# Performance work log

Measured on AMD Instinct MI355X. Metric: run time of the kernel, lower is better.

The kernel has to match this reference:

```python
import jax, jax.numpy as jnp
import numpy as np

WINDOW = 5  # len_sort_window in the original module


def setup_inputs() -> dict:
    key = jax.random.key(0)
    k1, k2, k3 = jax.random.split(key, 3)
    B, L, D = 8, 4000, 512  # L divisible by WINDOW, D < L
    q = jax.random.normal(k1, (B, L, D), dtype=jnp.float32)
    k = jax.random.normal(k2, (B, L, D), dtype=jnp.float32)
    v = jax.random.normal(k3, (B, L, D), dtype=jnp.float32)
    return {"q": q, "k": k, "v": v}


def reference(q, k, v):
    # q, k are unused by the original forward.
    B, L, D = v.shape
    t = jnp.arange(L)          # sequence positions
    s = jnp.arange(D)          # per-feature cyclic shift amount (= feature index)
    # Shift feature i left by i: shifted[:, t, i] = v[:, (t + i) % L, i]
    idx_fwd = (t[:, None] + s[None, :]) % L            # [L, D]
    v_shift = jnp.take_along_axis(v, idx_fwd[None, :, :], axis=1)  # [B, L, D]
    # Sort within fixed non-overlapping windows of size WINDOW along the seq axis.
    v_sorted = jnp.sort(v_shift.reshape(B, L // WINDOW, WINDOW, D), axis=2)
    v_sorted = v_sorted.reshape(B, L, D)
    # Unshift feature i right by i: out[:, t, i] = v_sorted[:, (t - i) % L, i]
    idx_bwd = (t[:, None] - s[None, :]) % L            # [L, D]
    return jnp.take_along_axis(v_sorted, idx_bwd[None, :, :], axis=1)
```

## Files before the change

### kernel.cpp

```cpp
#include <hip/hip_runtime.h>


constexpr int L   = 4000;
constexpr int D   = 512;
constexpr int NW  = L / 5;
constexpr int WPB = 2;
constexpr int NBX = NW / WPB;

typedef float f4 __attribute__((ext_vector_type(4)));

#define CE(a, b) { float lo_ = fminf(a, b); float hi_ = fmaxf(a, b); (a) = lo_; (b) = hi_; }

__global__ __launch_bounds__(256, 4)
void swd18_asmld(const float* __restrict__ v, float* __restrict__ out) {
    const int nwg = gridDim.x * gridDim.y;
    const int lid = blockIdx.x + gridDim.x * blockIdx.y;
    const int qq  = nwg >> 3;
    const int xcd = lid & 7;
    const int pos = lid >> 3;
    const int nid = xcd * qq + pos;

    const int b  = nid / NBX;
    const int bx = nid % NBX;

    const int w  = WPB * bx + (threadIdx.x >> 7);
    const int q  = threadIdx.x & 127;
    const int c0 = q << 2;
    const int R0 = 5 * w;

    const f4* __restrict__ vb4 = (const f4*)(v   + (size_t)b * (L * D));
    f4*       __restrict__ ob4 = (f4*)      (out + (size_t)b * (L * D));

    f4 in[14];
#pragma unroll
    for (int r = 0; r < 14; ++r) {
        int row = R0 - 5 + r;
        if (row < 0)  row += L;
        if (row >= L) row -= L;
        const f4* p = vb4 + (size_t)row * (D / 4) + q;
        asm volatile("global_load_dwordx4 %0, %1, off"
                     : "=&v"(in[r]) : "v"(p));
    }
    asm volatile("s_waitcnt vmcnt(0)" ::: "memory");
    __builtin_amdgcn_sched_barrier(0);

    const int rc0 = c0 % 5;
    f4 o0, o1, o2, o3, o4;

#define COMP(J, F) do {                                                         \
    int rcj = rc0 + (J); if (rcj >= 5) rcj -= 5;                                \
    const bool e0 = rcj == 0, e1 = rcj == 1, e2 = rcj == 2, e3 = rcj == 3;      \
    float A0 = e0 ? in[0].F : e1 ? in[1].F : e2 ? in[2].F : e3 ? in[3].F : in[4].F;   \
    float A1 = e0 ? in[1].F : e1 ? in[2].F : e2 ? in[3].F : e3 ? in[4].F : in[5].F;   \
    float A2 = e0 ? in[2].F : e1 ? in[3].F : e2 ? in[4].F : e3 ? in[5].F : in[6].F;   \
    float A3 = e0 ? in[3].F : e1 ? in[4].F : e2 ? in[5].F : e3 ? in[6].F : in[7].F;   \
    float A4 = e0 ? in[4].F : e1 ? in[5].F : e2 ? in[6].F : e3 ? in[7].F : in[8].F;   \
    float B0 = e0 ? in[5].F : e1 ? in[6].F : e2 ? in[7].F : e3 ? in[8].F : in[9].F;   \
    float B1 = e0 ? in[6].F : e1 ? in[7].F : e2 ? in[8].F : e3 ? in[9].F : in[10].F;  \
    float B2 = e0 ? in[7].F : e1 ? in[8].F : e2 ? in[9].F : e3 ? in[10].F : in[11].F; \
    float B3 = e0 ? in[8].F : e1 ? in[9].F : e2 ? in[10].F : e3 ? in[11].F : in[12].F;\
    float B4 = e0 ? in[9].F : e1 ? in[10].F : e2 ? in[11].F : e3 ? in[12].F : in[13].F;\
    CE(A0, A1) CE(A3, A4) CE(A2, A4) CE(A2, A3) CE(A1, A4)                      \
    CE(A0, A3) CE(A0, A2) CE(A1, A3) CE(A1, A2)                                 \
    CE(B0, B1) CE(B3, B4) CE(B2, B4) CE(B2, B3) CE(B1, B4)                      \
    CE(B0, B3) CE(B0, B2) CE(B1, B3) CE(B1, B2)                                 \
    o0.F = e0 ? B0 : e1 ? A4 : e2 ? A3 : e3 ? A2 : A1;                          \
    o1.F = e0 ? B1 : e1 ? B0 : e2 ? A4 : e3 ? A3 : A2;                          \
    o2.F = e0 ? B2 : e1 ? B1 : e2 ? B0 : e3 ? A4 : A3;                          \
    o3.F = e0 ? B3 : e1 ? B2 : e2 ? B1 : e3 ? B0 : A4;                          \
    o4.F = e0 ? B4 : e1 ? B3 : e2 ? B2 : e3 ? B1 : B0;                          \
} while (0)

    COMP(0, x);
    COMP(1, y);
    COMP(2, z);
    COMP(3, w);
#undef COMP

    f4* o = ob4 + (size_t)R0 * (D / 4) + q;
    __builtin_nontemporal_store(o0, o + 0 * (D / 4));
    __builtin_nontemporal_store(o1, o + 1 * (D / 4));
    __builtin_nontemporal_store(o2, o + 2 * (D / 4));
    __builtin_nontemporal_store(o3, o + 3 * (D / 4));
    __builtin_nontemporal_store(o4, o + 4 * (D / 4));
}

#undef CE

extern "C" void kernel_launch(void* const* d_in, const int* in_sizes, int n_in,
                              void* d_out, int out_size, void* d_ws, size_t ws_size,
                              hipStream_t stream) {
    const float* v = (const float*)d_in[2];
    float* out = (float*)d_out;

    const int B = in_sizes[2] / (L * D);
    dim3 grid(NBX, B);
    swd18_asmld<<<grid, dim3(256), 0, stream>>>(v, out);
}
```

Before: 184.3 us.

## Process 25-row strips per thread with float2 columns to cut halo reloads

Each thread now covers a strip of five consecutive 5-row output groups across two feature columns instead of one group across four columns. It loads 34 input rows instead of 14 per group, so the halo rows needed by the per-column shift are shared across groups. The goal is to reduce redundant global reads. The cost is fewer blocks, narrower dwordx2 loads and a larger per-thread register set.

```diff
diff --git a/kernel.cpp b/kernel.cpp
--- a/kernel.cpp
+++ b/kernel.cpp
@@ -1,18 +1,19 @@
 #include <hip/hip_runtime.h>
 
 
-constexpr int L   = 4000;
-constexpr int D   = 512;
-constexpr int NW  = L / 5;
-constexpr int WPB = 2;
-constexpr int NBX = NW / WPB;
+constexpr int L    = 4000;
+constexpr int D    = 512;
+constexpr int G    = 5;
+constexpr int SR   = 5 * G;
+constexpr int NSTR = L / SR;
+constexpr int NR   = SR + 9;
 
-typedef float f4 __attribute__((ext_vector_type(4)));
+typedef float f2 __attribute__((ext_vector_type(2)));
 
 #define CE(a, b) { float lo_ = fminf(a, b); float hi_ = fmaxf(a, b); (a) = lo_; (b) = hi_; }
 
 __global__ __launch_bounds__(256, 4)
-void swd18_asmld(const float* __restrict__ v, float* __restrict__ out) {
+void swd18_f2g5(const float* __restrict__ v, float* __restrict__ out) {
     const int nwg = gridDim.x * gridDim.y;
     const int lid = blockIdx.x + gridDim.x * blockIdx.y;
     const int qq  = nwg >> 3;
@@ -20,46 +21,42 @@
     const int pos = lid >> 3;
     const int nid = xcd * qq + pos;
 
-    const int b  = nid / NBX;
-    const int bx = nid % NBX;
+    const int b     = nid / NSTR;
+    const int strip = nid % NSTR;
+    const int t     = threadIdx.x;
+    const int R0    = strip * SR;
 
-    const int w  = WPB * bx + (threadIdx.x >> 7);
-    const int q  = threadIdx.x & 127;
-    const int c0 = q << 2;
-    const int R0 = 5 * w;
+    const f2* __restrict__ vb2 = (const f2*)(v   + (size_t)b * (L * D));
+    f2*       __restrict__ ob2 = (f2*)      (out + (size_t)b * (L * D));
 
-    const f4* __restrict__ vb4 = (const f4*)(v   + (size_t)b * (L * D));
-    f4*       __restrict__ ob4 = (f4*)      (out + (size_t)b * (L * D));
-
-    f4 in[14];
+    f2 in[NR];
 #pragma unroll
-    for (int r = 0; r < 14; ++r) {
+    for (int r = 0; r < NR; ++r) {
         int row = R0 - 5 + r;
         if (row < 0)  row += L;
         if (row >= L) row -= L;
-        const f4* p = vb4 + (size_t)row * (D / 4) + q;
-        asm volatile("global_load_dwordx4 %0, %1, off"
+        const f2* p = vb2 + (size_t)row * (D / 2) + t;
+        asm volatile("global_load_dwordx2 %0, %1, off"
                      : "=&v"(in[r]) : "v"(p));
     }
     asm volatile("s_waitcnt vmcnt(0)" ::: "memory");
     __builtin_amdgcn_sched_barrier(0);
 
-    const int rc0 = c0 % 5;
-    f4 o0, o1, o2, o3, o4;
+    const int rc0 = (2 * t) % 5;
 
-#define COMP(J, F) do {                                                         \
+#define COMP(WB, J, F) do {                                                     \
     int rcj = rc0 + (J); if (rcj >= 5) rcj -= 5;                                \
     const bool e0 = rcj == 0, e1 = rcj == 1, e2 = rcj == 2, e3 = rcj == 3;      \
-    float A0 = e0 ? in[0].F : e1 ? in[1].F : e2 ? in[2].F : e3 ? in[3].F : in[4].F;   \
-    float A1 = e0 ? in[1].F : e1 ? in[2].F : e2 ? in[3].F : e3 ? in[4].F : in[5].F;   \
-    float A2 = e0 ? in[2].F : e1 ? in[3].F : e2 ? in[4].F : e3 ? in[5].F : in[6].F;   \
-    float A3 = e0 ? in[3].F : e1 ? in[4].F : e2 ? in[5].F : e3 ? in[6].F : in[7].F;   \
-    float A4 = e0 ? in[4].F : e1 ? in[5].F : e2 ? in[6].F : e3 ? in[7].F : in[8].F;   \
-    float B0 = e0 ? in[5].F : e1 ? in[6].F : e2 ? in[7].F : e3 ? in[8].F : in[9].F;   \
-    float B1 = e0 ? in[6].F : e1 ? in[7].F : e2 ? in[8].F : e3 ? in[9].F : in[10].F;  \
-    float B2 = e0 ? in[7].F : e1 ? in[8].F : e2 ? in[9].F : e3 ? in[10].F : in[11].F; \
-    float B3 = e0 ? in[8].F : e1 ? in[9].F : e2 ? in[10].F : e3 ? in[11].F : in[12].F;\
-    float B4 = e0 ? in[9].F : e1 ? in[10].F : e2 ? in[11].F : e3 ? in[12].F : in[13].F;\
+    float A0 = e0 ? in[(WB)+0].F : e1 ? in[(WB)+1].F : e2 ? in[(WB)+2].F : e3 ? in[(WB)+3].F : in[(WB)+4].F;    \
+    float A1 = e0 ? in[(WB)+1].F : e1 ? in[(WB)+2].F : e2 ? in[(WB)+3].F : e3 ? in[(WB)+4].F : in[(WB)+5].F;    \
+    float A2 = e0 ? in[(WB)+2].F : e1 ? in[(WB)+3].F : e2 ? in[(WB)+4].F : e3 ? in[(WB)+5].F : in[(WB)+6].F;    \
+    float A3 = e0 ? in[(WB)+3].F : e1 ? in[(WB)+4].F : e2 ? in[(WB)+5].F : e3 ? in[(WB)+6].F : in[(WB)+7].F;    \
+    float A4 = e0 ? in[(WB)+4].F : e1 ? in[(WB)+5].F : e2 ? in[(WB)+6].F : e3 ? in[(WB)+7].F : in[(WB)+8].F;    \
+    float B0 = e0 ? in[(WB)+5].F : e1 ? in[(WB)+6].F : e2 ? in[(WB)+7].F : e3 ? in[(WB)+8].F : in[(WB)+9].F;    \
+    float B1 = e0 ? in[(WB)+6].F : e1 ? in[(WB)+7].F : e2 ? in[(WB)+8].F : e3 ? in[(WB)+9].F : in[(WB)+10].F;   \
+    float B2 = e0 ? in[(WB)+7].F : e1 ? in[(WB)+8].F : e2 ? in[(WB)+9].F : e3 ? in[(WB)+10].F : in[(WB)+11].F;  \
+    float B3 = e0 ? in[(WB)+8].F : e1 ? in[(WB)+9].F : e2 ? in[(WB)+10].F : e3 ? in[(WB)+11].F : in[(WB)+12].F; \
+    float B4 = e0 ? in[(WB)+9].F : e1 ? in[(WB)+10].F : e2 ? in[(WB)+11].F : e3 ? in[(WB)+12].F : in[(WB)+13].F;\
     CE(A0, A1) CE(A3, A4) CE(A2, A4) CE(A2, A3) CE(A1, A4)                      \
     CE(A0, A3) CE(A0, A2) CE(A1, A3) CE(A1, A2)                                 \
     CE(B0, B1) CE(B3, B4) CE(B2, B4) CE(B2, B3) CE(B1, B4)                      \
@@ -71,18 +68,20 @@
     o4.F = e0 ? B4 : e1 ? B3 : e2 ? B2 : e3 ? B1 : B0;                          \
 } while (0)
 
-    COMP(0, x);
-    COMP(1, y);
-    COMP(2, z);
-    COMP(3, w);
+#pragma unroll
+    for (int k = 0; k < G; ++k) {
+        f2 o0, o1, o2, o3, o4;
+        COMP(5 * k, 0, x);
+        COMP(5 * k, 1, y);
+
+        f2* o = ob2 + (size_t)(R0 + 5 * k) * (D / 2) + t;
+        __builtin_nontemporal_store(o0, o + 0 * (D / 2));
+        __builtin_nontemporal_store(o1, o + 1 * (D / 2));
+        __builtin_nontemporal_store(o2, o + 2 * (D / 2));
+        __builtin_nontemporal_store(o3, o + 3 * (D / 2));
+        __builtin_nontemporal_store(o4, o + 4 * (D / 2));
+    }
 #undef COMP
-
-    f4* o = ob4 + (size_t)R0 * (D / 4) + q;
-    __builtin_nontemporal_store(o0, o + 0 * (D / 4));
-    __builtin_nontemporal_store(o1, o + 1 * (D / 4));
-    __builtin_nontemporal_store(o2, o + 2 * (D / 4));
-    __builtin_nontemporal_store(o3, o + 3 * (D / 4));
-    __builtin_nontemporal_store(o4, o + 4 * (D / 4));
 }
 
 #undef CE
@@ -94,6 +93,6 @@
     float* out = (float*)d_out;
 
     const int B = in_sizes[2] / (L * D);
-    dim3 grid(NBX, B);
-    swd18_asmld<<<grid, dim3(256), 0, stream>>>(v, out);
+    dim3 grid(NSTR, B);
+    swd18_f2g5<<<grid, dim3(256), 0, stream>>>(v, out);
 }
```

After: 177.0 us. -4.0%, faster.
